# Performance work log

Hardware: AMD Instinct MI355X
Metric: run time of the kernel (lower is better)

## Reference

```python
import jax, jax.numpy as jnp
import numpy as np

N = 1_000_000   # detections
FDIM = 64       # embedding dim
C = 128         # number of clusters (track ids in [0, C))
DELTA_VAR = 0.5
DELTA_DIST = 3.0


def setup_inputs() -> dict:
    key = jax.random.key(0)
    k1, k2 = jax.random.split(key)
    features = jax.random.normal(k1, (N, FDIM), dtype=jnp.float32)
    labels = jax.random.randint(k2, (N, 2), 0, C, dtype=jnp.int32)  # [fr, track_id], all ids >= 0
    return {"features": features, "labels": labels}


def reference(features, labels):
    # All track ids are >= 0 by construction, so the tp_ids filter is a no-op
    # and the dynamic unique-cluster loop becomes a fixed-C segment reduce.
    ids = labels[:, 1]
    ones = jnp.ones((features.shape[0],), dtype=features.dtype)
    counts = jax.ops.segment_sum(ones, ids, num_segments=C)            # (C,)
    sums = jax.ops.segment_sum(features, ids, num_segments=C)         # (C, F)
    means = sums / counts[:, None]                                     # per-cluster mean

    # variance term: per-point distance to its cluster mean, hinged at delta_var
    d = jnp.linalg.norm(features - means[ids], axis=1)                 # (N,)
    per_pt = jnp.square(jax.nn.relu(d - DELTA_VAR))
    per_cluster = jax.ops.segment_sum(per_pt, ids, num_segments=C) / counts
    var_loss = jnp.sum(per_cluster) / C

    # pairwise cluster-distance term over i != j, hinged at delta_dist
    diff = means[:, None, :] - means[None, :, :]                       # (C, C, F)
    sq = jnp.sum(diff * diff, axis=-1)                                 # (C, C)
    eye = jnp.eye(C, dtype=bool)
    pd = jnp.sqrt(jnp.where(eye, 1.0, sq))                             # safe sqrt on diagonal
    dl = jnp.where(eye, 0.0, jnp.square(jax.nn.relu(DELTA_DIST - pd)))
    dist_loss = jnp.sum(dl) / (C * (C - 1))

    return var_loss + dist_loss
```

## Files before the change

### kernel.cpp

```cpp
#include <hip/hip_runtime.h>

#define NPTS 1000000
#define FDIM 64
#define CNUM 128
#define PSTRIDE 8320
#define NB1 1024
#define NB3 1024

typedef _Float16 half8 __attribute__((ext_vector_type(8)));
typedef float f32x4 __attribute__((ext_vector_type(4)));

__global__ __launch_bounds__(256, 4) void k1_partials(
    const float* __restrict__ feats, const int* __restrict__ labels,
    float* __restrict__ partials, int nblocks)
{
    __shared__ float lds[FDIM * 132];
    __shared__ float cnt[CNUM];
    const int tid = threadIdx.x;
    if (tid < CNUM) cnt[tid] = 0.f;
    __syncthreads();

    const int lane = tid & 63;
    const int n15 = lane & 15;
    const int kb = (lane >> 4) * 8;
    const int rowb = (lane >> 4) * 4;
    const int w = tid >> 6;
    const int fh = w & 1;
    const int fbase = fh * 32;
    const int nstreams = nblocks * 2;
    const int ts = ((blockIdx.x << 2) + w) >> 1;

    f32x4 acc[8][2];
    #pragma unroll
    for (int ct = 0; ct < 8; ++ct)
        #pragma unroll
        for (int nt = 0; nt < 2; ++nt)
            acc[ct][nt] = (f32x4){0.f, 0.f, 0.f, 0.f};

    const int ntiles = NPTS / 32;
    for (int t = ts; t < ntiles; t += nstreams) {
        const int p0 = t * 32;
        const float* fp = feats + (size_t)(p0 + kb) * FDIM + fbase + n15;
        const int* lp = labels + 2 * (p0 + kb) + 1;
        int vlab[8];
        #pragma unroll
        for (int i = 0; i < 8; ++i) vlab[i] = lp[2 * i];

        half8 B[2];
        #pragma unroll
        for (int nt = 0; nt < 2; ++nt) {
            #pragma unroll
            for (int i = 0; i < 8; ++i)
                B[nt][i] = (_Float16)fp[i * FDIM + nt * 16];
        }
        if (fh == 0 && lane < 32) {
            const int myl = labels[2 * (p0 + lane) + 1];
            atomicAdd(&cnt[myl], 1.0f);
        }
        #pragma unroll
        for (int ct = 0; ct < 8; ++ct) {
            const int cmine = ct * 16 + n15;
            union { unsigned u[4]; half8 h; } ua;
            #pragma unroll
            for (int j = 0; j < 4; ++j)
                ua.u[j] = ((vlab[2 * j] == cmine) ? 0x3C00u : 0u)
                        | ((vlab[2 * j + 1] == cmine) ? 0x3C000000u : 0u);
            #pragma unroll
            for (int nt = 0; nt < 2; ++nt)
                acc[ct][nt] = __builtin_amdgcn_mfma_f32_16x16x32_f16(
                    ua.h, B[nt], acc[ct][nt], 0, 0, 0);
        }
    }
    __syncthreads();

    for (int r = 0; r < 2; ++r) {
        if ((w >> 1) == r) {
            #pragma unroll
            for (int ct = 0; ct < 8; ++ct)
                #pragma unroll
                for (int nt = 0; nt < 2; ++nt) {
                    float* a = &lds[(fbase + nt * 16 + n15) * 132 + ct * 16 + rowb];
                    if (r == 0) *(f32x4*)a = acc[ct][nt];
                    else        *(f32x4*)a = *(f32x4*)a + acc[ct][nt];
                }
        }
        __syncthreads();
    }

    float* dst = partials + (size_t)blockIdx.x * PSTRIDE;
    for (int i4 = tid; i4 < 2048; i4 += 256) {
        const int f = i4 >> 5, c0 = (i4 & 31) * 4;
        __builtin_nontemporal_store(*(const f32x4*)&lds[f * 132 + c0],
                                    (f32x4*)dst + i4);
    }
    if (tid < CNUM)
        __builtin_nontemporal_store(cnt[tid], &dst[8192 + tid]);
}

__global__ __launch_bounds__(256) void k2_reduce(
    const float* __restrict__ partials, int nblocks, float* __restrict__ red,
    float* __restrict__ ppsum, float* __restrict__ dsum, int* __restrict__ counter)
{
    const int tid = threadIdx.x;
    const int tsub = tid & 31, grp = tid >> 5;
    const int t0 = blockIdx.x * 32;
    float s = 0.f;
    #pragma unroll 8
    for (int b = grp; b < nblocks; b += 8)
        s += __builtin_nontemporal_load(&partials[(size_t)b * PSTRIDE + t0 + tsub]);
    __shared__ float lred[8][33];
    lred[grp][tsub] = s;
    __syncthreads();
    if (tid < 32) {
        float tot = 0.f;
        #pragma unroll
        for (int q = 0; q < 8; ++q) tot += lred[q][tid];
        const int t = t0 + tid;
        if (t < 8192) red[(t & 127) * FDIM + (t >> 7)] = tot;
        else red[t] = tot;
    }
    if (blockIdx.x == 0) {
        if (tid >= 128) ppsum[tid - 128] = 0.f;
        if (tid == 64) dsum[0] = 0.f;
        if (tid == 65) counter[0] = 0;
    }
}

__global__ __launch_bounds__(256, 4) void k3_var(
    const float4* __restrict__ feats4, const int* __restrict__ labels,
    const float* __restrict__ red, float* __restrict__ ppsum, int nblocks)
{
    __shared__ float4 mu4[CNUM * 16];
    __shared__ float lpp[CNUM];
    const int tid = threadIdx.x;
    for (int i = tid; i < 2048; i += 256) {
        float4 sv = ((const float4*)red)[i];
        float ci = 1.0f / red[8192 + (i >> 4)];
        mu4[i] = make_float4(sv.x * ci, sv.y * ci, sv.z * ci, sv.w * ci);
    }
    if (tid < CNUM) lpp[tid] = 0.f;
    __syncthreads();

    const int lane = tid & 63;
    const int k = lane & 15, g = lane >> 4;
    const int nwaves = nblocks * 4;
    const int wid = ((blockIdx.x << 8) + tid) >> 6;
    const int ntiles = NPTS / 16;

    int b = ntiles - 1 - wid;
    float4 v[4]; int cc = 0;
    if (b >= 0) {
        const float4* fp = feats4 + (size_t)b * 256 + lane;
        #pragma unroll
        for (int s = 0; s < 4; ++s) v[s] = fp[s * 64];
        cc = labels[2 * (b * 16 + k) + 1];
    }
    while (b >= 0) {
        const int bn = b - nwaves;
        float4 vn[4]; int ccn = 0;
        if (bn >= 0) {
            const float4* fp = feats4 + (size_t)bn * 256 + lane;
            #pragma unroll
            for (int s = 0; s < 4; ++s) vn[s] = fp[s * 64];
            ccn = labels[2 * (bn * 16 + k) + 1];
        }
        #pragma unroll
        for (int s = 0; s < 4; ++s) {
            const int c = __shfl(cc, 4 * s + g);
            float4 m = mu4[c * 16 + k];
            float dx = v[s].x - m.x, dy = v[s].y - m.y,
                  dz = v[s].z - m.z, dw = v[s].w - m.w;
            float sq = dx * dx + dy * dy + dz * dz + dw * dw;
            sq += __shfl_xor(sq, 1); sq += __shfl_xor(sq, 2);
            sq += __shfl_xor(sq, 4); sq += __shfl_xor(sq, 8);
            if (k == 0) {
                const float t = sqrtf(sq) - 0.5f;
                if (t > 0.f) atomicAdd(&lpp[c], t * t);
            }
        }
        b = bn;
        #pragma unroll
        for (int s = 0; s < 4; ++s) v[s] = vn[s];
        cc = ccn;
    }
    __syncthreads();
    if (tid < CNUM) atomicAdd(&ppsum[tid], lpp[tid]);
}

__global__ __launch_bounds__(128) void k45_dist_final(
    const float* __restrict__ red, const float* __restrict__ ppsum,
    float* __restrict__ dsum, int* __restrict__ counter, float* __restrict__ out)
{
    __shared__ float4 mu4[CNUM * 17];
    __shared__ int lastflag;
    __shared__ float sv[2];
    const int tid = threadIdx.x;
    for (int i = tid; i < 2048; i += 128) {
        float4 s4 = ((const float4*)red)[i];
        float ci = 1.0f / red[8192 + (i >> 4)];
        mu4[(i >> 4) * 17 + (i & 15)] =
            make_float4(s4.x * ci, s4.y * ci, s4.z * ci, s4.w * ci);
    }
    __syncthreads();
    const int i = blockIdx.x, j = tid;
    float sq = 0.f;
    #pragma unroll
    for (int q = 0; q < 16; ++q) {
        float4 a = mu4[i * 17 + q], b = mu4[j * 17 + q];
        float dx = a.x - b.x, dy = a.y - b.y, dz = a.z - b.z, dw = a.w - b.w;
        sq += dx * dx + dy * dy + dz * dz + dw * dw;
    }
    float dl = 0.f;
    if (j != i) {
        const float r = 3.0f - sqrtf(sq);
        if (r > 0.f) dl = r * r;
    }
    #pragma unroll
    for (int m = 1; m < 64; m <<= 1) dl += __shfl_xor(dl, m);
    if ((tid & 63) == 0) atomicAdd(dsum, dl);
    __threadfence();
    __syncthreads();
    if (tid == 0) lastflag = (atomicAdd(counter, 1) == (int)gridDim.x - 1);
    __syncthreads();
    if (lastflag) {
        float v = ppsum[tid] / red[8192 + tid];
        #pragma unroll
        for (int m = 1; m < 64; m <<= 1) v += __shfl_xor(v, m);
        if ((tid & 63) == 0) sv[tid >> 6] = v;
    }
    __syncthreads();
    if (lastflag && tid == 0) {
        const float dtot = atomicAdd(dsum, 0.0f);
        out[0] = (sv[0] + sv[1]) / (float)CNUM
               + dtot / (float)(CNUM * (CNUM - 1));
    }
}

extern "C" void kernel_launch(void* const* d_in, const int* in_sizes, int n_in,
                              void* d_out, int out_size, void* d_ws, size_t ws_size,
                              hipStream_t stream) {
    (void)in_sizes; (void)n_in; (void)out_size;
    const float* feats   = (const float*)d_in[0];
    const float4* feats4 = (const float4*)d_in[0];
    const int* labels    = (const int*)d_in[1];
    float* ws            = (float*)d_ws;
    float* out           = (float*)d_out;

    int nb1 = NB1;
    {
        size_t avail = ws_size / sizeof(float);
        size_t fixed = PSTRIDE + 128 + 2;
        if (avail > fixed) {
            size_t cap = (avail - fixed) / PSTRIDE;
            if ((size_t)nb1 > cap) nb1 = (int)cap;
        } else nb1 = 1;
        if (nb1 < 1) nb1 = 1;
    }
    float* partials = ws;
    float* red      = ws + (size_t)nb1 * PSTRIDE;
    float* ppsum    = red + PSTRIDE;
    float* dsum     = ppsum + 128;
    int*   counter  = (int*)(dsum + 1);

    k1_partials<<<nb1, 256, 0, stream>>>(feats, labels, partials, nb1);
    k2_reduce<<<PSTRIDE / 32, 256, 0, stream>>>(partials, nb1, red, ppsum, dsum, counter);
    k3_var<<<NB3, 256, 0, stream>>>(feats4, labels, red, ppsum, NB3);
    k45_dist_final<<<CNUM, 128, 0, stream>>>(red, ppsum, dsum, counter, out);
}
```

Before: 132.6 us.

## Cache fp16 copy of features in k1 and read it in variance pass

```diff
diff --git a/kernel.cpp b/kernel.cpp
--- a/kernel.cpp
+++ b/kernel.cpp
@@ -8,11 +8,12 @@
 #define NB3 1024
 
 typedef _Float16 half8 __attribute__((ext_vector_type(8)));
+typedef _Float16 half2v __attribute__((ext_vector_type(2)));
 typedef float f32x4 __attribute__((ext_vector_type(4)));
 
 __global__ __launch_bounds__(256, 4) void k1_partials(
     const float* __restrict__ feats, const int* __restrict__ labels,
-    float* __restrict__ partials, int nblocks)
+    float* __restrict__ partials, half2v* __restrict__ f16c, int nblocks)
 {
     __shared__ float lds[FDIM * 132];
     __shared__ float cnt[CNUM];
@@ -48,10 +49,12 @@
 
         half8 B[2];
         #pragma unroll
-        for (int nt = 0; nt < 2; ++nt) {
-            #pragma unroll
-            for (int i = 0; i < 8; ++i)
-                B[nt][i] = (_Float16)fp[i * FDIM + nt * 16];
+        for (int i = 0; i < 8; ++i) {
+            const float f0 = fp[i * FDIM];
+            const float f1 = fp[i * FDIM + 16];
+            half2v wv; wv[0] = (_Float16)f0; wv[1] = (_Float16)f1;
+            B[0][i] = wv[0]; B[1][i] = wv[1];
+            f16c[(size_t)(p0 + kb + i) * 32 + fh * 16 + n15] = wv;
         }
         if (fh == 0 && lane < 32) {
             const int myl = labels[2 * (p0 + lane) + 1];
@@ -127,53 +130,61 @@
 }
 
 __global__ __launch_bounds__(256, 4) void k3_var(
-    const float4* __restrict__ feats4, const int* __restrict__ labels,
+    const half8* __restrict__ f16c, const int* __restrict__ labels,
     const float* __restrict__ red, float* __restrict__ ppsum, int nblocks)
 {
-    __shared__ float4 mu4[CNUM * 16];
+    __shared__ float mu[CNUM * 68];
     __shared__ float lpp[CNUM];
     const int tid = threadIdx.x;
-    for (int i = tid; i < 2048; i += 256) {
-        float4 sv = ((const float4*)red)[i];
-        float ci = 1.0f / red[8192 + (i >> 4)];
-        mu4[i] = make_float4(sv.x * ci, sv.y * ci, sv.z * ci, sv.w * ci);
+    for (int idx = tid; idx < CNUM * 32; idx += 256) {
+        const int c = idx >> 5, q = idx & 31;
+        const int flo = ((q >> 4) << 5) + (q & 15);
+        const float inv = 1.0f / red[8192 + c];
+        mu[c * 68 + q * 2]     = red[c * 64 + flo] * inv;
+        mu[c * 68 + q * 2 + 1] = red[c * 64 + flo + 16] * inv;
     }
     if (tid < CNUM) lpp[tid] = 0.f;
     __syncthreads();
 
     const int lane = tid & 63;
-    const int k = lane & 15, g = lane >> 4;
+    const int l8 = lane & 7, pgrp = lane >> 3;
     const int nwaves = nblocks * 4;
     const int wid = ((blockIdx.x << 8) + tid) >> 6;
-    const int ntiles = NPTS / 16;
+    const int ntiles = NPTS / 32;
 
     int b = ntiles - 1 - wid;
-    float4 v[4]; int cc = 0;
+    half8 v[4]; int cc = 0;
     if (b >= 0) {
-        const float4* fp = feats4 + (size_t)b * 256 + lane;
+        const half8* fp = f16c + (size_t)b * 256 + lane;
         #pragma unroll
         for (int s = 0; s < 4; ++s) v[s] = fp[s * 64];
-        cc = labels[2 * (b * 16 + k) + 1];
+        cc = labels[2 * (b * 32 + (lane & 31)) + 1];
     }
     while (b >= 0) {
         const int bn = b - nwaves;
-        float4 vn[4]; int ccn = 0;
+        half8 vn[4]; int ccn = 0;
         if (bn >= 0) {
-            const float4* fp = feats4 + (size_t)bn * 256 + lane;
+            const half8* fp = f16c + (size_t)bn * 256 + lane;
             #pragma unroll
             for (int s = 0; s < 4; ++s) vn[s] = fp[s * 64];
-            ccn = labels[2 * (bn * 16 + k) + 1];
+            ccn = labels[2 * (bn * 32 + (lane & 31)) + 1];
         }
         #pragma unroll
         for (int s = 0; s < 4; ++s) {
-            const int c = __shfl(cc, 4 * s + g);
-            float4 m = mu4[c * 16 + k];
-            float dx = v[s].x - m.x, dy = v[s].y - m.y,
-                  dz = v[s].z - m.z, dw = v[s].w - m.w;
-            float sq = dx * dx + dy * dy + dz * dz + dw * dw;
-            sq += __shfl_xor(sq, 1); sq += __shfl_xor(sq, 2);
-            sq += __shfl_xor(sq, 4); sq += __shfl_xor(sq, 8);
-            if (k == 0) {
+            const int c = __shfl(cc, 8 * s + pgrp);
+            const float* m = &mu[c * 68 + l8 * 8];
+            const f32x4 m0 = *(const f32x4*)m;
+            const f32x4 m1 = *(const f32x4*)(m + 4);
+            float d0 = (float)v[s][0] - m0[0], d1 = (float)v[s][1] - m0[1];
+            float d2 = (float)v[s][2] - m0[2], d3 = (float)v[s][3] - m0[3];
+            float sq = d0 * d0 + d1 * d1 + d2 * d2 + d3 * d3;
+            d0 = (float)v[s][4] - m1[0]; d1 = (float)v[s][5] - m1[1];
+            d2 = (float)v[s][6] - m1[2]; d3 = (float)v[s][7] - m1[3];
+            sq += d0 * d0 + d1 * d1 + d2 * d2 + d3 * d3;
+            sq += __shfl_xor(sq, 1);
+            sq += __shfl_xor(sq, 2);
+            sq += __shfl_xor(sq, 4);
+            if (l8 == 0) {
                 const float t = sqrtf(sq) - 0.5f;
                 if (t > 0.f) atomicAdd(&lpp[c], t * t);
             }
@@ -241,17 +252,16 @@
                               hipStream_t stream) {
     (void)in_sizes; (void)n_in; (void)out_size;
     const float* feats   = (const float*)d_in[0];
-    const float4* feats4 = (const float4*)d_in[0];
     const int* labels    = (const int*)d_in[1];
     float* ws            = (float*)d_ws;
     float* out           = (float*)d_out;
 
+    const size_t f16_bytes = (size_t)NPTS * 32 * sizeof(half2v);
     int nb1 = NB1;
     {
-        size_t avail = ws_size / sizeof(float);
-        size_t fixed = PSTRIDE + 128 + 2;
-        if (avail > fixed) {
-            size_t cap = (avail - fixed) / PSTRIDE;
+        const size_t tail = (size_t)(PSTRIDE + 130) * 4 + 32 + f16_bytes;
+        if (ws_size > tail) {
+            size_t cap = (ws_size - tail) / ((size_t)PSTRIDE * 4);
             if ((size_t)nb1 > cap) nb1 = (int)cap;
         } else nb1 = 1;
         if (nb1 < 1) nb1 = 1;
@@ -261,9 +271,11 @@
     float* ppsum    = red + PSTRIDE;
     float* dsum     = ppsum + 128;
     int*   counter  = (int*)(dsum + 1);
-
-    k1_partials<<<nb1, 256, 0, stream>>>(feats, labels, partials, nb1);
+    const size_t fixed_bytes = ((size_t)nb1 * PSTRIDE + PSTRIDE + 128 + 2) * 4;
+    half2v* f16c = (half2v*)((char*)d_ws + ((fixed_bytes + 15) & ~(size_t)15));
+
+    k1_partials<<<nb1, 256, 0, stream>>>(feats, labels, partials, f16c, nb1);
     k2_reduce<<<PSTRIDE / 32, 256, 0, stream>>>(partials, nb1, red, ppsum, dsum, counter);
-    k3_var<<<NB3, 256, 0, stream>>>(feats4, labels, red, ppsum, NB3);
+    k3_var<<<NB3, 256, 0, stream>>>((const half8*)f16c, labels, red, ppsum, NB3);
     k45_dist_final<<<CNUM, 128, 0, stream>>>(red, ppsum, dsum, counter, out);
 }
```

Result: slower. 186.0 us (+40.3%).

## Stage feature tiles through LDS with coalesced float4 loads and register prefetch

Applied to the files above, without the earlier changes.

```diff
diff --git a/kernel.cpp b/kernel.cpp
--- a/kernel.cpp
+++ b/kernel.cpp
@@ -3,6 +3,7 @@
 #define NPTS 1000000
 #define FDIM 64
 #define CNUM 128
+#define NTILES 31250
 #define PSTRIDE 8320
 #define NB1 1024
 #define NB3 1024
@@ -11,88 +12,102 @@
 typedef float f32x4 __attribute__((ext_vector_type(4)));
 
 __global__ __launch_bounds__(256, 4) void k1_partials(
-    const float* __restrict__ feats, const int* __restrict__ labels,
+    const float4* __restrict__ feats4, const int* __restrict__ labels,
     float* __restrict__ partials, int nblocks)
 {
-    __shared__ float lds[FDIM * 132];
+    __shared__ float tile[32][66];
     __shared__ float cnt[CNUM];
     const int tid = threadIdx.x;
     if (tid < CNUM) cnt[tid] = 0.f;
-    __syncthreads();
 
     const int lane = tid & 63;
     const int n15 = lane & 15;
-    const int kb = (lane >> 4) * 8;
-    const int rowb = (lane >> 4) * 4;
+    const int g = lane >> 4;
+    const int kb = g * 8;
+    const int rowb = g * 4;
     const int w = tid >> 6;
-    const int fh = w & 1;
+    const int fh = w & 1, ch = w >> 1;
     const int fbase = fh * 32;
-    const int nstreams = nblocks * 2;
-    const int ts = ((blockIdx.x << 2) + w) >> 1;
-
-    f32x4 acc[8][2];
-    #pragma unroll
-    for (int ct = 0; ct < 8; ++ct)
+    const int cbase = ch * 64;
+    const int pr0 = w * 8 + g;
+    const int c4 = n15 * 4;
+
+    f32x4 acc[4][2];
+    #pragma unroll
+    for (int ct = 0; ct < 4; ++ct)
         #pragma unroll
         for (int nt = 0; nt < 2; ++nt)
             acc[ct][nt] = (f32x4){0.f, 0.f, 0.f, 0.f};
 
-    const int ntiles = NPTS / 32;
-    for (int t = ts; t < ntiles; t += nstreams) {
+    int t = blockIdx.x;
+    float4 r0, r1; int vl[8]; int cl = 0;
+    if (t < NTILES) {
         const int p0 = t * 32;
-        const float* fp = feats + (size_t)(p0 + kb) * FDIM + fbase + n15;
+        r0 = feats4[(size_t)(p0 + pr0) * 16 + n15];
+        r1 = feats4[(size_t)(p0 + pr0 + 4) * 16 + n15];
         const int* lp = labels + 2 * (p0 + kb) + 1;
-        int vlab[8];
-        #pragma unroll
-        for (int i = 0; i < 8; ++i) vlab[i] = lp[2 * i];
+        #pragma unroll
+        for (int i = 0; i < 8; ++i) vl[i] = lp[2 * i];
+        if (w == 0 && lane < 32) cl = labels[2 * (p0 + lane) + 1];
+    }
+    __syncthreads();
+
+    while (t < NTILES) {
+        *(f32x4*)&tile[pr0][c4]     = *(const f32x4*)&r0;
+        *(f32x4*)&tile[pr0 + 4][c4] = *(const f32x4*)&r1;
+        __syncthreads();
+
+        const int tn = t + nblocks;
+        float4 q0, q1; int vl2[8]; int cl2 = 0;
+        if (tn < NTILES) {
+            const int p0 = tn * 32;
+            q0 = feats4[(size_t)(p0 + pr0) * 16 + n15];
+            q1 = feats4[(size_t)(p0 + pr0 + 4) * 16 + n15];
+            const int* lp = labels + 2 * (p0 + kb) + 1;
+            #pragma unroll
+            for (int i = 0; i < 8; ++i) vl2[i] = lp[2 * i];
+            if (w == 0 && lane < 32) cl2 = labels[2 * (p0 + lane) + 1];
+        }
+        if (w == 0 && lane < 32) atomicAdd(&cnt[cl], 1.0f);
 
         half8 B[2];
         #pragma unroll
-        for (int nt = 0; nt < 2; ++nt) {
-            #pragma unroll
-            for (int i = 0; i < 8; ++i)
-                B[nt][i] = (_Float16)fp[i * FDIM + nt * 16];
-        }
-        if (fh == 0 && lane < 32) {
-            const int myl = labels[2 * (p0 + lane) + 1];
-            atomicAdd(&cnt[myl], 1.0f);
-        }
-        #pragma unroll
-        for (int ct = 0; ct < 8; ++ct) {
-            const int cmine = ct * 16 + n15;
+        for (int i = 0; i < 8; ++i) {
+            B[0][i] = (_Float16)tile[kb + i][fbase + n15];
+            B[1][i] = (_Float16)tile[kb + i][fbase + 16 + n15];
+        }
+        #pragma unroll
+        for (int ct = 0; ct < 4; ++ct) {
+            const int cmine = cbase + ct * 16 + n15;
             union { unsigned u[4]; half8 h; } ua;
             #pragma unroll
             for (int j = 0; j < 4; ++j)
-                ua.u[j] = ((vlab[2 * j] == cmine) ? 0x3C00u : 0u)
-                        | ((vlab[2 * j + 1] == cmine) ? 0x3C000000u : 0u);
+                ua.u[j] = ((vl[2 * j] == cmine) ? 0x3C00u : 0u)
+                        | ((vl[2 * j + 1] == cmine) ? 0x3C000000u : 0u);
             #pragma unroll
             for (int nt = 0; nt < 2; ++nt)
                 acc[ct][nt] = __builtin_amdgcn_mfma_f32_16x16x32_f16(
                     ua.h, B[nt], acc[ct][nt], 0, 0, 0);
         }
-    }
-    __syncthreads();
-
-    for (int r = 0; r < 2; ++r) {
-        if ((w >> 1) == r) {
-            #pragma unroll
-            for (int ct = 0; ct < 8; ++ct)
-                #pragma unroll
-                for (int nt = 0; nt < 2; ++nt) {
-                    float* a = &lds[(fbase + nt * 16 + n15) * 132 + ct * 16 + rowb];
-                    if (r == 0) *(f32x4*)a = acc[ct][nt];
-                    else        *(f32x4*)a = *(f32x4*)a + acc[ct][nt];
-                }
-        }
         __syncthreads();
+        t = tn;
+        r0 = q0; r1 = q1;
+        #pragma unroll
+        for (int i = 0; i < 8; ++i) vl[i] = vl2[i];
+        cl = cl2;
     }
 
     float* dst = partials + (size_t)blockIdx.x * PSTRIDE;
-    for (int i4 = tid; i4 < 2048; i4 += 256) {
-        const int f = i4 >> 5, c0 = (i4 & 31) * 4;
-        __builtin_nontemporal_store(*(const f32x4*)&lds[f * 132 + c0],
-                                    (f32x4*)dst + i4);
-    }
+    #pragma unroll
+    for (int ct = 0; ct < 4; ++ct)
+        #pragma unroll
+        for (int nt = 0; nt < 2; ++nt)
+            #pragma unroll
+            for (int reg = 0; reg < 4; ++reg) {
+                const int c = cbase + ct * 16 + rowb + reg;
+                const int f = fbase + nt * 16 + n15;
+                __builtin_nontemporal_store(acc[ct][nt][reg], &dst[c * FDIM + f]);
+            }
     if (tid < CNUM)
         __builtin_nontemporal_store(cnt[tid], &dst[8192 + tid]);
 }
@@ -115,9 +130,7 @@
         float tot = 0.f;
         #pragma unroll
         for (int q = 0; q < 8; ++q) tot += lred[q][tid];
-        const int t = t0 + tid;
-        if (t < 8192) red[(t & 127) * FDIM + (t >> 7)] = tot;
-        else red[t] = tot;
+        red[t0 + tid] = tot;
     }
     if (blockIdx.x == 0) {
         if (tid >= 128) ppsum[tid - 128] = 0.f;
@@ -240,7 +253,6 @@
                               void* d_out, int out_size, void* d_ws, size_t ws_size,
                               hipStream_t stream) {
     (void)in_sizes; (void)n_in; (void)out_size;
-    const float* feats   = (const float*)d_in[0];
     const float4* feats4 = (const float4*)d_in[0];
     const int* labels    = (const int*)d_in[1];
     float* ws            = (float*)d_ws;
@@ -262,7 +274,7 @@
     float* dsum     = ppsum + 128;
     int*   counter  = (int*)(dsum + 1);
 
-    k1_partials<<<nb1, 256, 0, stream>>>(feats, labels, partials, nb1);
+    k1_partials<<<nb1, 256, 0, stream>>>(feats4, labels, partials, nb1);
     k2_reduce<<<PSTRIDE / 32, 256, 0, stream>>>(partials, nb1, red, ppsum, dsum, counter);
     k3_var<<<NB3, 256, 0, stream>>>(feats4, labels, red, ppsum, NB3);
     k45_dist_final<<<CNUM, 128, 0, stream>>>(red, ppsum, dsum, counter, out);
```

Measured after the change: 134.2 us. About the same (+1.2%).

## Store per-block partial sums in fp16 and raise block counts

Applied to the files above, without the earlier changes.

```diff
diff --git a/kernel.cpp b/kernel.cpp
--- a/kernel.cpp
+++ b/kernel.cpp
@@ -4,17 +4,18 @@
 #define FDIM 64
 #define CNUM 128
 #define PSTRIDE 8320
-#define NB1 1024
-#define NB3 1024
+#define NB1 1536
+#define NB3 1536
 
 typedef _Float16 half8 __attribute__((ext_vector_type(8)));
+typedef _Float16 half4v __attribute__((ext_vector_type(4)));
 typedef float f32x4 __attribute__((ext_vector_type(4)));
 
 __global__ __launch_bounds__(256, 4) void k1_partials(
     const float* __restrict__ feats, const int* __restrict__ labels,
-    float* __restrict__ partials, int nblocks)
-{
-    __shared__ float lds[FDIM * 132];
+    _Float16* __restrict__ partials, int nblocks)
+{
+    __shared__ _Float16 ldsH[FDIM * 132];
     __shared__ float cnt[CNUM];
     const int tid = threadIdx.x;
     if (tid < CNUM) cnt[tid] = 0.f;
@@ -41,10 +42,13 @@
     for (int t = ts; t < ntiles; t += nstreams) {
         const int p0 = t * 32;
         const float* fp = feats + (size_t)(p0 + kb) * FDIM + fbase + n15;
-        const int* lp = labels + 2 * (p0 + kb) + 1;
+        const int4* lq = (const int4*)(labels + 2 * (p0 + kb));
         int vlab[8];
-        #pragma unroll
-        for (int i = 0; i < 8; ++i) vlab[i] = lp[2 * i];
+        {
+            int4 a0 = lq[0], a1 = lq[1], a2 = lq[2], a3 = lq[3];
+            vlab[0] = a0.y; vlab[1] = a0.w; vlab[2] = a1.y; vlab[3] = a1.w;
+            vlab[4] = a2.y; vlab[5] = a2.w; vlab[6] = a3.y; vlab[7] = a3.w;
+        }
 
         half8 B[2];
         #pragma unroll
@@ -79,26 +83,40 @@
             for (int ct = 0; ct < 8; ++ct)
                 #pragma unroll
                 for (int nt = 0; nt < 2; ++nt) {
-                    float* a = &lds[(fbase + nt * 16 + n15) * 132 + ct * 16 + rowb];
-                    if (r == 0) *(f32x4*)a = acc[ct][nt];
-                    else        *(f32x4*)a = *(f32x4*)a + acc[ct][nt];
+                    _Float16* a = &ldsH[(fbase + nt * 16 + n15) * 132 + ct * 16 + rowb];
+                    half4v h;
+                    if (r == 0) {
+                        #pragma unroll
+                        for (int q = 0; q < 4; ++q) h[q] = (_Float16)acc[ct][nt][q];
+                    } else {
+                        half4v o = *(const half4v*)a;
+                        #pragma unroll
+                        for (int q = 0; q < 4; ++q)
+                            h[q] = (_Float16)((float)o[q] + acc[ct][nt][q]);
+                    }
+                    *(half4v*)a = h;
                 }
         }
         __syncthreads();
     }
 
-    float* dst = partials + (size_t)blockIdx.x * PSTRIDE;
-    for (int i4 = tid; i4 < 2048; i4 += 256) {
-        const int f = i4 >> 5, c0 = (i4 & 31) * 4;
-        __builtin_nontemporal_store(*(const f32x4*)&lds[f * 132 + c0],
-                                    (f32x4*)dst + i4);
-    }
-    if (tid < CNUM)
-        __builtin_nontemporal_store(cnt[tid], &dst[8192 + tid]);
+    _Float16* dst = partials + (size_t)blockIdx.x * PSTRIDE;
+    for (int i8 = tid; i8 < 1040; i8 += 256) {
+        half8 v;
+        if (i8 < 1024) {
+            const int f = i8 >> 4, c0 = (i8 & 15) * 8;
+            v = *(const half8*)&ldsH[f * 132 + c0];
+        } else {
+            const int c0 = (i8 - 1024) * 8;
+            #pragma unroll
+            for (int q = 0; q < 8; ++q) v[q] = (_Float16)cnt[c0 + q];
+        }
+        __builtin_nontemporal_store(v, (half8*)dst + i8);
+    }
 }
 
 __global__ __launch_bounds__(256) void k2_reduce(
-    const float* __restrict__ partials, int nblocks, float* __restrict__ red,
+    const _Float16* __restrict__ partials, int nblocks, float* __restrict__ red,
     float* __restrict__ ppsum, float* __restrict__ dsum, int* __restrict__ counter)
 {
     const int tid = threadIdx.x;
@@ -107,7 +125,8 @@
     float s = 0.f;
     #pragma unroll 8
     for (int b = grp; b < nblocks; b += 8)
-        s += __builtin_nontemporal_load(&partials[(size_t)b * PSTRIDE + t0 + tsub]);
+        s += (float)__builtin_nontemporal_load(
+                 &partials[(size_t)b * PSTRIDE + t0 + tsub]);
     __shared__ float lred[8][33];
     lred[grp][tsub] = s;
     __syncthreads();
@@ -126,7 +145,7 @@
     }
 }
 
-__global__ __launch_bounds__(256, 4) void k3_var(
+__global__ __launch_bounds__(256, 6) void k3_var(
     const float4* __restrict__ feats4, const int* __restrict__ labels,
     const float* __restrict__ red, float* __restrict__ ppsum, int nblocks)
 {
@@ -243,21 +262,19 @@
     const float* feats   = (const float*)d_in[0];
     const float4* feats4 = (const float4*)d_in[0];
     const int* labels    = (const int*)d_in[1];
-    float* ws            = (float*)d_ws;
     float* out           = (float*)d_out;
 
     int nb1 = NB1;
     {
-        size_t avail = ws_size / sizeof(float);
-        size_t fixed = PSTRIDE + 128 + 2;
-        if (avail > fixed) {
-            size_t cap = (avail - fixed) / PSTRIDE;
+        const size_t tail = (size_t)(PSTRIDE + 130) * 4;
+        if (ws_size > tail) {
+            size_t cap = (ws_size - tail) / ((size_t)PSTRIDE * sizeof(_Float16));
             if ((size_t)nb1 > cap) nb1 = (int)cap;
         } else nb1 = 1;
         if (nb1 < 1) nb1 = 1;
     }
-    float* partials = ws;
-    float* red      = ws + (size_t)nb1 * PSTRIDE;
+    _Float16* partials = (_Float16*)d_ws;
+    float* red      = (float*)((char*)d_ws + (size_t)nb1 * PSTRIDE * 2);
     float* ppsum    = red + PSTRIDE;
     float* dsum     = ppsum + 128;
     int*   counter  = (int*)(dsum + 1);
```

Measured after the change: 139.8 us. 5.4% more time.
